# Performance work log

Measured on AMD Instinct MI355X. Metric: run time of the kernel, lower is better.

## Reference

```python
import jax, jax.numpy as jnp
import numpy as np

CODEBOOK_SIZE = 8192
EMBED_DIM = 256


def setup_inputs() -> dict:
    key = jax.random.key(0)
    k1, k2 = jax.random.split(key)
    z = jax.random.normal(k1, (8, 4096, EMBED_DIM), dtype=jnp.float32)
    # matches torch init: uniform_(-1/codebook_size, 1/codebook_size)
    codebook = jax.random.uniform(
        k2, (CODEBOOK_SIZE, EMBED_DIM), dtype=jnp.float32,
        minval=-1.0 / CODEBOOK_SIZE, maxval=1.0 / CODEBOOK_SIZE)
    return {"z": z, "codebook": codebook}


def reference(z, codebook):
    # z: [B, S, D]; codebook: [K, D]
    z_flat = z.reshape(-1, z.shape[-1])                      # [N, D]
    # ||z||^2 - 2 z.E^T + ||E||^2  -> [N, K]
    distances = (
        jnp.sum(z_flat * z_flat, axis=1, keepdims=True)
        - 2.0 * jnp.einsum("nd,kd->nk", z_flat, codebook)
        + jnp.sum(codebook * codebook, axis=1)
    )
    encoding_indices = jnp.argmin(distances, axis=1)         # [N]
    z_q = codebook[encoding_indices].reshape(z.shape)        # [B, S, D]
    return z_q, encoding_indices
```

## Files before the change

### kernel.cpp

```cpp
#include <hip/hip_runtime.h>


#define NROWS 32768
#define DIM   256
#define KCB   8192
#define CANDCAP 128
#define MARGIN  4.5e-4f
#define WBUF    320

#define SB_CAND  0u
#define SB_CNT   8388608u
#define SB_ZSQ   8519680u
#define SB_CSQ   8650752u
#define SB_CSQ1  8683520u
#define SB_OVL   8716288u
#define SB_OVC   8847360u
#define SB_IMG   8847424u
#define SB_NEED  13041728u

using bf16x8 = __attribute__((ext_vector_type(8))) short;
using f32x4  = __attribute__((ext_vector_type(4))) float;

__device__ __forceinline__ unsigned short bf16rne(float f) {
    unsigned u = __float_as_uint(f);
    unsigned r = u + 0x7FFFu + ((u >> 16) & 1u);
    return (unsigned short)(r >> 16);
}

__device__ float np_sumsq_256(const float* __restrict__ p) {
#pragma clang fp contract(off)
    float blk[2];
    #pragma unroll
    for (int b = 0; b < 2; ++b) {
        const float4* q4 = reinterpret_cast<const float4*>(p + b * 128);
        float4 a0 = q4[0], a1 = q4[1];
        float r[8];
        r[0] = __fmul_rn(a0.x, a0.x); r[1] = __fmul_rn(a0.y, a0.y);
        r[2] = __fmul_rn(a0.z, a0.z); r[3] = __fmul_rn(a0.w, a0.w);
        r[4] = __fmul_rn(a1.x, a1.x); r[5] = __fmul_rn(a1.y, a1.y);
        r[6] = __fmul_rn(a1.z, a1.z); r[7] = __fmul_rn(a1.w, a1.w);
        #pragma unroll
        for (int i = 2; i < 32; i += 2) {
            a0 = q4[i]; a1 = q4[i + 1];
            r[0] = __fadd_rn(r[0], __fmul_rn(a0.x, a0.x));
            r[1] = __fadd_rn(r[1], __fmul_rn(a0.y, a0.y));
            r[2] = __fadd_rn(r[2], __fmul_rn(a0.z, a0.z));
            r[3] = __fadd_rn(r[3], __fmul_rn(a0.w, a0.w));
            r[4] = __fadd_rn(r[4], __fmul_rn(a1.x, a1.x));
            r[5] = __fadd_rn(r[5], __fmul_rn(a1.y, a1.y));
            r[6] = __fadd_rn(r[6], __fmul_rn(a1.z, a1.z));
            r[7] = __fadd_rn(r[7], __fmul_rn(a1.w, a1.w));
        }
        blk[b] = __fadd_rn(
            __fadd_rn(__fadd_rn(r[0], r[1]), __fadd_rn(r[2], r[3])),
            __fadd_rn(__fadd_rn(r[4], r[5]), __fadd_rn(r[6], r[7])));
    }
    return __fadd_rn(blk[0], blk[1]);
}

__global__ void vq_prep_kernel(const float* __restrict__ z,
                               const float* __restrict__ cb,
                               char* __restrict__ img,
                               float* __restrict__ zsq, float* __restrict__ csq,
                               float* __restrict__ csq1,
                               unsigned* __restrict__ cnt, unsigned* __restrict__ ovc) {
    int t = blockIdx.x * 256 + threadIdx.x;
    if (t < NROWS) cnt[t] = 0;
    if (t == 0) *ovc = 0;
    if (t < 262144) {
        int s = t & 63, kk = (t >> 6) & 7, T = t >> 9;
        int code = s & 15, lhi = s >> 4;
        const float* src = cb + (size_t)(T * 16 + code) * DIM + kk * 32 + lhi * 8;
        float4 v0 = *reinterpret_cast<const float4*>(src);
        float4 v1 = *reinterpret_cast<const float4*>(src + 4);
        uint4 o;
        o.x = (unsigned)bf16rne(v0.x) | ((unsigned)bf16rne(v0.y) << 16);
        o.y = (unsigned)bf16rne(v0.z) | ((unsigned)bf16rne(v0.w) << 16);
        o.z = (unsigned)bf16rne(v1.x) | ((unsigned)bf16rne(v1.y) << 16);
        o.w = (unsigned)bf16rne(v1.z) | ((unsigned)bf16rne(v1.w) << 16);
        *reinterpret_cast<uint4*>(img + (size_t)T * 8192 + kk * 1024 + s * 16) = o;
    } else if (t < 262144 + KCB) {
        int k = t - 262144;
        float s = np_sumsq_256(cb + (size_t)k * DIM);
        csq[k] = s;
        csq1[k] = s + 1.0f;
    } else if (t < 262144 + KCB + NROWS) {
        int r = t - 262144 - KCB;
        zsq[r] = np_sumsq_256(z + (size_t)r * DIM);
    }
}

__global__ __launch_bounds__(512, 2) void vq_screen_kernel(
    const float* __restrict__ z, const char* __restrict__ img,
    const float* __restrict__ csq1,
    unsigned* __restrict__ cnt, unsigned short* __restrict__ cand) {
    __shared__ unsigned runmin[128];
    __shared__ unsigned wcnt[8];
    __shared__ unsigned wbuf[8][WBUF];
    const int tid = threadIdx.x, lane = tid & 63, wid = tid >> 6;
    const int wr = wid >> 2, wc = wid & 3;
    const int l15 = lane & 15, lhi = lane >> 4;
    const int row0 = blockIdx.x * 128;
    const int tbase = wc * 128;

    bf16x8 ah[4][8];
    #pragma unroll
    for (int m = 0; m < 4; ++m) {
        const float* zr = z + (size_t)(row0 + wr * 64 + m * 16 + l15) * DIM;
        #pragma unroll
        for (int kk = 0; kk < 8; ++kk) {
            float4 v0 = *reinterpret_cast<const float4*>(zr + kk * 32 + lhi * 8);
            float4 v1 = *reinterpret_cast<const float4*>(zr + kk * 32 + lhi * 8 + 4);
            uint4 o;
            o.x = (unsigned)bf16rne(v0.x) | ((unsigned)bf16rne(v0.y) << 16);
            o.y = (unsigned)bf16rne(v0.z) | ((unsigned)bf16rne(v0.w) << 16);
            o.z = (unsigned)bf16rne(v1.x) | ((unsigned)bf16rne(v1.y) << 16);
            o.w = (unsigned)bf16rne(v1.z) | ((unsigned)bf16rne(v1.w) << 16);
            ah[m][kk] = __builtin_bit_cast(bf16x8, o);
        }
    }

    if (tid < 128) runmin[tid] = 0x7F800000u;
    if (tid < 8) wcnt[tid] = 0;
    __syncthreads();

    f32x4 acc[4];
    #pragma unroll
    for (int m = 0; m < 4; ++m) acc[m] = (f32x4){0.f, 0.f, 0.f, 0.f};

    const char*  gp = img + (size_t)tbase * 8192 + (size_t)lane * 16;
    const float* cp = csq1 + tbase * 16 + l15;
    int codeb = tbase * 16 + l15;

    uint4 bA[8]; float csA;
    uint4 bB[8]; float csB;

    auto PUSH = [&](int lr, int code) {
        unsigned pi = atomicAdd(&wcnt[wid], 1u);
        if (pi < WBUF) wbuf[wid][pi] = ((unsigned)lr << 13) | (unsigned)code;
        else {
            int grow = row0 + lr;
            unsigned gs = atomicAdd(&cnt[grow], 1u);
            if (gs < CANDCAP) cand[(size_t)grow * CANDCAP + gs] = (unsigned short)code;
        }
    };

#define CHUNKS(bcur, bnxt, csn, DOLOAD)                                   \
    {                                                                     \
        _Pragma("unroll")                                                 \
        for (int c = 0; c < 4; ++c) {                                     \
            if (DOLOAD) {                                                 \
                bnxt[2*c]   = *reinterpret_cast<const uint4*>(gp + (2*c) * 1024);     \
                bnxt[2*c+1] = *reinterpret_cast<const uint4*>(gp + (2*c+1) * 1024);   \
                if (c == 0) csn = *cp;                                    \
            }                                                             \
            bf16x8 b0 = __builtin_bit_cast(bf16x8, bcur[2*c]);            \
            bf16x8 b1 = __builtin_bit_cast(bf16x8, bcur[2*c+1]);          \
            _Pragma("unroll")                                             \
            for (int m = 0; m < 4; ++m)                                   \
                acc[m] = __builtin_amdgcn_mfma_f32_16x16x32_bf16(ah[m][2*c], b0, acc[m], 0, 0, 0);   \
            _Pragma("unroll")                                             \
            for (int m = 0; m < 4; ++m)                                   \
                acc[m] = __builtin_amdgcn_mfma_f32_16x16x32_bf16(ah[m][2*c+1], b1, acc[m], 0, 0, 0); \
        }                                                                 \
        if (DOLOAD) { gp += 8192; cp += 16; }                             \
    }

#define EPI(csv)                                                          \
    {                                                                     \
        _Pragma("unroll")                                                 \
        for (int m = 0; m < 4; ++m) {                                     \
            const int lr0 = wr * 64 + m * 16 + lhi * 4;                   \
            uint4 rmb = *reinterpret_cast<const uint4*>(&runmin[lr0]);    \
            float s0 = fmaf(acc[m][0], -2.0f, csv);                       \
            float s1 = fmaf(acc[m][1], -2.0f, csv);                       \
            float s2 = fmaf(acc[m][2], -2.0f, csv);                       \
            float s3 = fmaf(acc[m][3], -2.0f, csv);                       \
            bool c0 = s0 < __uint_as_float(rmb.x) + MARGIN;               \
            bool c1 = s1 < __uint_as_float(rmb.y) + MARGIN;               \
            bool c2 = s2 < __uint_as_float(rmb.z) + MARGIN;               \
            bool c3 = s3 < __uint_as_float(rmb.w) + MARGIN;               \
            if (__any(c0 | c1 | c2 | c3)) {                               \
                if (c0) { if (s0 < __uint_as_float(rmb.x)) atomicMin(&runmin[lr0 + 0], __float_as_uint(s0)); PUSH(lr0 + 0, codeb); } \
                if (c1) { if (s1 < __uint_as_float(rmb.y)) atomicMin(&runmin[lr0 + 1], __float_as_uint(s1)); PUSH(lr0 + 1, codeb); } \
                if (c2) { if (s2 < __uint_as_float(rmb.z)) atomicMin(&runmin[lr0 + 2], __float_as_uint(s2)); PUSH(lr0 + 2, codeb); } \
                if (c3) { if (s3 < __uint_as_float(rmb.w)) atomicMin(&runmin[lr0 + 3], __float_as_uint(s3)); PUSH(lr0 + 3, codeb); } \
            }                                                             \
            acc[m] = (f32x4){0.f, 0.f, 0.f, 0.f};                         \
        }                                                                 \
        codeb += 16;                                                      \
    }

    #pragma unroll
    for (int kk = 0; kk < 8; ++kk)
        bA[kk] = *reinterpret_cast<const uint4*>(gp + kk * 1024);
    csA = *cp; gp += 8192; cp += 16;

    CHUNKS(bA, bB, csB, 1);
    {
        #pragma unroll
        for (int m = 0; m < 4; ++m) {
            const int lr0 = wr * 64 + m * 16 + lhi * 4;
            #pragma unroll
            for (int r = 0; r < 4; ++r) {
                float s2 = fmaf(acc[m][r], -2.0f, csA);
                float sm = s2;
                sm = fminf(sm, __shfl_xor(sm, 1));
                sm = fminf(sm, __shfl_xor(sm, 2));
                sm = fminf(sm, __shfl_xor(sm, 4));
                sm = fminf(sm, __shfl_xor(sm, 8));
                if (l15 == 0) atomicMin(&runmin[lr0 + r], __float_as_uint(sm));
                if (s2 < sm + MARGIN) PUSH(lr0 + r, codeb);
            }
            acc[m] = (f32x4){0.f, 0.f, 0.f, 0.f};
        }
        codeb += 16;
    }
    CHUNKS(bB, bA, csA, 1);  EPI(csB);

    for (int t = 2; t < 126; t += 2) {
        CHUNKS(bA, bB, csB, 1);  EPI(csA);
        CHUNKS(bB, bA, csA, 1);  EPI(csB);
    }
    CHUNKS(bA, bB, csB, 1);  EPI(csA);
    CHUNKS(bB, bA, csA, 0);  EPI(csB);

    unsigned n = wcnt[wid]; if (n > WBUF) n = WBUF;
    for (unsigned e = lane; e < n; e += 64) {
        unsigned u = wbuf[wid][e];
        int row = row0 + (int)(u >> 13);
        int code = (int)(u & 8191u);
        unsigned slot = atomicAdd(&cnt[row], 1u);
        if (slot < CANDCAP) cand[(size_t)row * CANDCAP + slot] = (unsigned short)code;
    }
#undef CHUNKS
#undef EPI
}

__global__ __launch_bounds__(256) void vq_exact_kernel(
    const float* __restrict__ z, const float* __restrict__ cb,
    const float* __restrict__ zsq, const float* __restrict__ csq,
    const unsigned* __restrict__ cnt, const unsigned short* __restrict__ cand,
    unsigned* __restrict__ ovl, unsigned* __restrict__ ovc,
    float* __restrict__ idxF, float4* __restrict__ outz, int fused) {
    __shared__ float zrow[4][DIM];
    const int wid = threadIdx.x >> 6, lane = threadIdx.x & 63;
    const int row = blockIdx.x * 4 + wid;

    float4 zv4 = *reinterpret_cast<const float4*>(&z[(size_t)row * DIM + lane * 4]);
    *reinterpret_cast<float4*>(&zrow[wid][lane * 4]) = zv4;
    __syncthreads();

    const unsigned c = cnt[row];
    if (c == 0 || c > CANDCAP) {
        if (lane == 0) { unsigned s = atomicAdd(ovc, 1u); ovl[s] = row; }
        return;
    }

    const float Zr = zsq[row];
    const float4* cb4 = reinterpret_cast<const float4*>(cb);
    float best = 3.4e38f;
    int   bi   = 0x7FFFFFFF;

    for (int j = lane; j < (int)c; j += 64) {
        int k = cand[(size_t)row * CANDCAP + j];
        float a = 0.0f;
        #pragma unroll 8
        for (int q = 0; q < 64; ++q) {
            float4 cv = cb4[(size_t)k * 64 + q];
            float4 zv = *reinterpret_cast<const float4*>(&zrow[wid][q * 4]);
            a = fmaf(zv.x, cv.x, a); a = fmaf(zv.y, cv.y, a);
            a = fmaf(zv.z, cv.z, a); a = fmaf(zv.w, cv.w, a);
        }
        float sv = __fadd_rn(__fsub_rn(Zr, __fmul_rn(2.0f, a)), csq[k]);
        if (sv < best || (sv == best && k < bi)) { best = sv; bi = k; }
    }
    #pragma unroll
    for (int mk = 32; mk >= 1; mk >>= 1) {
        float ov = __shfl_xor(best, mk);
        int   oi = __shfl_xor(bi, mk);
        if (ov < best || (ov == best && oi < bi)) { best = ov; bi = oi; }
    }
    if (lane == 0) idxF[row] = (float)bi;
    if (fused) outz[(size_t)row * 64 + lane] = cb4[(size_t)bi * 64 + lane];
}

__global__ __launch_bounds__(256) void vq_cleanup_kernel(
    const float* __restrict__ z, const float* __restrict__ cb,
    const float* __restrict__ zsq, const float* __restrict__ csq,
    const unsigned* __restrict__ ovl, const unsigned* __restrict__ ovc,
    float* __restrict__ idxF, float4* __restrict__ outz, int fused) {
    __shared__ float zrow[DIM];
    __shared__ float wv[4]; __shared__ int wi[4];
    __shared__ int sbi;
    const int lane = threadIdx.x & 63, wid = threadIdx.x >> 6;
    const unsigned count = *ovc;
    for (unsigned w = blockIdx.x; w < count; w += gridDim.x) {
        const int row = ovl[w];
        __syncthreads();
        *reinterpret_cast<float4*>(&zrow[threadIdx.x * 4 & (DIM - 1)]) =
            *reinterpret_cast<const float4*>(&z[(size_t)row * DIM + (threadIdx.x * 4 & (DIM - 1))]);
        __syncthreads();
        const float Zr = zsq[row];
        const float4* cb4 = reinterpret_cast<const float4*>(cb);
        float best = 3.4e38f; int bi = 0x7FFFFFFF;
        for (int k = threadIdx.x; k < KCB; k += 256) {
            float a = 0.0f;
            #pragma unroll 8
            for (int q = 0; q < 64; ++q) {
                float4 cv = cb4[(size_t)k * 64 + q];
                float4 zv = *reinterpret_cast<const float4*>(&zrow[q * 4]);
                a = fmaf(zv.x, cv.x, a); a = fmaf(zv.y, cv.y, a);
                a = fmaf(zv.z, cv.z, a); a = fmaf(zv.w, cv.w, a);
            }
            float sv = __fadd_rn(__fsub_rn(Zr, __fmul_rn(2.0f, a)), csq[k]);
            if (sv < best || (sv == best && k < bi)) { best = sv; bi = k; }
        }
        #pragma unroll
        for (int mk = 32; mk >= 1; mk >>= 1) {
            float ov = __shfl_xor(best, mk);
            int   oi = __shfl_xor(bi, mk);
            if (ov < best || (ov == best && oi < bi)) { best = ov; bi = oi; }
        }
        if (lane == 0) { wv[wid] = best; wi[wid] = bi; }
        __syncthreads();
        if (threadIdx.x == 0) {
            #pragma unroll
            for (int u = 1; u < 4; ++u)
                if (wv[u] < best || (wv[u] == best && wi[u] < bi)) { best = wv[u]; bi = wi[u]; }
            idxF[row] = (float)bi;
            sbi = bi;
        }
        __syncthreads();
        if (fused && threadIdx.x < 64)
            outz[(size_t)row * 64 + threadIdx.x] = cb4[(size_t)sbi * 64 + threadIdx.x];
    }
}

__global__ void vq_gather_kernel(const float* __restrict__ cb,
                                 const float* __restrict__ idxF,
                                 float4* __restrict__ out4) {
    int g = blockIdx.x * blockDim.x + threadIdx.x;
    const float4* cb4 = reinterpret_cast<const float4*>(cb);
    for (int i = g; i < NROWS * 64; i += gridDim.x * blockDim.x) {
        int row = i >> 6, q = i & 63;
        int idx = (int)idxF[row];
        out4[i] = cb4[(size_t)idx * 64 + q];
    }
}

extern "C" void kernel_launch(void* const* d_in, const int* in_sizes, int n_in,
                              void* d_out, int out_size, void* d_ws, size_t ws_size,
                              hipStream_t stream) {
    const float* z  = (const float*)d_in[0];
    const float* cb = (const float*)d_in[1];
    float* out = (float*)d_out;

    const int fused = (ws_size >= (size_t)SB_NEED) ? 1 : 0;
    char* SB = fused ? (char*)d_ws : (char*)d_out;

    unsigned short* candp = (unsigned short*)(SB + SB_CAND);
    unsigned*       cntp  = (unsigned*)(SB + SB_CNT);
    float*          zsq   = (float*)(SB + SB_ZSQ);
    float*          csq   = (float*)(SB + SB_CSQ);
    float*          csq1  = (float*)(SB + SB_CSQ1);
    unsigned*       ovl   = (unsigned*)(SB + SB_OVL);
    unsigned*       ovc   = (unsigned*)(SB + SB_OVC);
    char*           img   = SB + SB_IMG;
    float*          idxF  = out + 8388608;

    vq_prep_kernel<<<(262144 + KCB + NROWS + 255) / 256, 256, 0, stream>>>(
        z, cb, img, zsq, csq, csq1, cntp, ovc);
    vq_screen_kernel<<<NROWS / 128, 512, 0, stream>>>(z, img, csq1, cntp, candp);
    vq_exact_kernel<<<NROWS / 4, 256, 0, stream>>>(
        z, cb, zsq, csq, cntp, candp, ovl, ovc, idxF, (float4*)out, fused);
    vq_cleanup_kernel<<<64, 256, 0, stream>>>(
        z, cb, zsq, csq, ovl, ovc, idxF, (float4*)out, fused);
    if (!fused)
        vq_gather_kernel<<<2048, 256, 0, stream>>>(cb, idxF, (float4*)out);
}
```

Before: 286.6 us.

## Double-buffer MFMA accumulators to overlap screening epilogue with next tile's MFMAs

The screen kernel's main loop now keeps two accumulator sets and two B-register buffers. Each step issues the MFMAs for one code tile while the epilogue (threshold compare, atomics, candidate push) runs on the previous tile's accumulators, so matrix work can overlap the scalar/LDS epilogue. The csq1 load moves into the epilogue and a bf16 pack helper is factored out. The extra accumulator registers raise VGPR pressure under launch_bounds(512,2) and could cause spilling.

```diff
diff --git a/kernel.cpp b/kernel.cpp
--- a/kernel.cpp
+++ b/kernel.cpp
@@ -20,11 +20,16 @@
 
 using bf16x8 = __attribute__((ext_vector_type(8))) short;
 using f32x4  = __attribute__((ext_vector_type(4))) float;
+using u32x4  = __attribute__((ext_vector_type(4))) unsigned int;
 
 __device__ __forceinline__ unsigned short bf16rne(float f) {
     unsigned u = __float_as_uint(f);
     unsigned r = u + 0x7FFFu + ((u >> 16) & 1u);
     return (unsigned short)(r >> 16);
+}
+
+__device__ __forceinline__ unsigned pack2_bf16(float a, float b) {
+    return (unsigned)bf16rne(a) | ((unsigned)bf16rne(b) << 16);
 }
 
 __device__ float np_sumsq_256(const float* __restrict__ p) {
@@ -74,10 +79,8 @@
         float4 v0 = *reinterpret_cast<const float4*>(src);
         float4 v1 = *reinterpret_cast<const float4*>(src + 4);
         uint4 o;
-        o.x = (unsigned)bf16rne(v0.x) | ((unsigned)bf16rne(v0.y) << 16);
-        o.y = (unsigned)bf16rne(v0.z) | ((unsigned)bf16rne(v0.w) << 16);
-        o.z = (unsigned)bf16rne(v1.x) | ((unsigned)bf16rne(v1.y) << 16);
-        o.w = (unsigned)bf16rne(v1.z) | ((unsigned)bf16rne(v1.w) << 16);
+        o.x = pack2_bf16(v0.x, v0.y); o.y = pack2_bf16(v0.z, v0.w);
+        o.z = pack2_bf16(v1.x, v1.y); o.w = pack2_bf16(v1.z, v1.w);
         *reinterpret_cast<uint4*>(img + (size_t)T * 8192 + kk * 1024 + s * 16) = o;
     } else if (t < 262144 + KCB) {
         int k = t - 262144;
@@ -112,10 +115,8 @@
             float4 v0 = *reinterpret_cast<const float4*>(zr + kk * 32 + lhi * 8);
             float4 v1 = *reinterpret_cast<const float4*>(zr + kk * 32 + lhi * 8 + 4);
             uint4 o;
-            o.x = (unsigned)bf16rne(v0.x) | ((unsigned)bf16rne(v0.y) << 16);
-            o.y = (unsigned)bf16rne(v0.z) | ((unsigned)bf16rne(v0.w) << 16);
-            o.z = (unsigned)bf16rne(v1.x) | ((unsigned)bf16rne(v1.y) << 16);
-            o.w = (unsigned)bf16rne(v1.z) | ((unsigned)bf16rne(v1.w) << 16);
+            o.x = pack2_bf16(v0.x, v0.y); o.y = pack2_bf16(v0.z, v0.w);
+            o.z = pack2_bf16(v1.x, v1.y); o.w = pack2_bf16(v1.z, v1.w);
             ah[m][kk] = __builtin_bit_cast(bf16x8, o);
         }
     }
@@ -124,16 +125,18 @@
     if (tid < 8) wcnt[tid] = 0;
     __syncthreads();
 
-    f32x4 acc[4];
+    f32x4 aA[4], aB[4];
     #pragma unroll
-    for (int m = 0; m < 4; ++m) acc[m] = (f32x4){0.f, 0.f, 0.f, 0.f};
-
-    const char*  gp = img + (size_t)tbase * 8192 + (size_t)lane * 16;
-    const float* cp = csq1 + tbase * 16 + l15;
+    for (int m = 0; m < 4; ++m) {
+        aA[m] = (f32x4){0.f, 0.f, 0.f, 0.f};
+        aB[m] = (f32x4){0.f, 0.f, 0.f, 0.f};
+    }
+
+    const char*  gp  = img + (size_t)tbase * 8192 + (size_t)lane * 16;
+    const float* cpe = csq1 + tbase * 16 + l15;
     int codeb = tbase * 16 + l15;
 
-    uint4 bA[8]; float csA;
-    uint4 bB[8]; float csB;
+    u32x4 bA[8], bB[8];
 
     auto PUSH = [&](int lr, int code) {
         unsigned pi = atomicAdd(&wcnt[wid], 1u);
@@ -145,37 +148,37 @@
         }
     };
 
-#define CHUNKS(bcur, bnxt, csn, DOLOAD)                                   \
+#define LOADR(bh)                                                         \
     {                                                                     \
         _Pragma("unroll")                                                 \
-        for (int c = 0; c < 4; ++c) {                                     \
-            if (DOLOAD) {                                                 \
-                bnxt[2*c]   = *reinterpret_cast<const uint4*>(gp + (2*c) * 1024);     \
-                bnxt[2*c+1] = *reinterpret_cast<const uint4*>(gp + (2*c+1) * 1024);   \
-                if (c == 0) csn = *cp;                                    \
-            }                                                             \
-            bf16x8 b0 = __builtin_bit_cast(bf16x8, bcur[2*c]);            \
-            bf16x8 b1 = __builtin_bit_cast(bf16x8, bcur[2*c+1]);          \
+        for (int kk = 0; kk < 8; ++kk)                                    \
+            bh[kk] = *reinterpret_cast<const u32x4*>(gp + kk * 1024);     \
+        gp += 8192;                                                       \
+    }
+
+#define MFMAS(bh, a)                                                      \
+    {                                                                     \
+        _Pragma("unroll")                                                 \
+        for (int kk = 0; kk < 8; ++kk) {                                  \
+            bf16x8 bv = __builtin_bit_cast(bf16x8, bh[kk]);               \
             _Pragma("unroll")                                             \
             for (int m = 0; m < 4; ++m)                                   \
-                acc[m] = __builtin_amdgcn_mfma_f32_16x16x32_bf16(ah[m][2*c], b0, acc[m], 0, 0, 0);   \
-            _Pragma("unroll")                                             \
-            for (int m = 0; m < 4; ++m)                                   \
-                acc[m] = __builtin_amdgcn_mfma_f32_16x16x32_bf16(ah[m][2*c+1], b1, acc[m], 0, 0, 0); \
+                a[m] = __builtin_amdgcn_mfma_f32_16x16x32_bf16(           \
+                    ah[m][kk], bv, a[m], 0, 0, 0);                        \
         }                                                                 \
-        if (DOLOAD) { gp += 8192; cp += 16; }                             \
-    }
-
-#define EPI(csv)                                                          \
+    }
+
+#define EPI(a)                                                            \
     {                                                                     \
+        const float csv = *cpe; cpe += 16;                                \
         _Pragma("unroll")                                                 \
         for (int m = 0; m < 4; ++m) {                                     \
             const int lr0 = wr * 64 + m * 16 + lhi * 4;                   \
             uint4 rmb = *reinterpret_cast<const uint4*>(&runmin[lr0]);    \
-            float s0 = fmaf(acc[m][0], -2.0f, csv);                       \
-            float s1 = fmaf(acc[m][1], -2.0f, csv);                       \
-            float s2 = fmaf(acc[m][2], -2.0f, csv);                       \
-            float s3 = fmaf(acc[m][3], -2.0f, csv);                       \
+            float s0 = fmaf(a[m][0], -2.0f, csv);                         \
+            float s1 = fmaf(a[m][1], -2.0f, csv);                         \
+            float s2 = fmaf(a[m][2], -2.0f, csv);                         \
+            float s3 = fmaf(a[m][3], -2.0f, csv);                         \
             bool c0 = s0 < __uint_as_float(rmb.x) + MARGIN;               \
             bool c1 = s1 < __uint_as_float(rmb.y) + MARGIN;               \
             bool c2 = s2 < __uint_as_float(rmb.z) + MARGIN;               \
@@ -186,24 +189,24 @@
                 if (c2) { if (s2 < __uint_as_float(rmb.z)) atomicMin(&runmin[lr0 + 2], __float_as_uint(s2)); PUSH(lr0 + 2, codeb); } \
                 if (c3) { if (s3 < __uint_as_float(rmb.w)) atomicMin(&runmin[lr0 + 3], __float_as_uint(s3)); PUSH(lr0 + 3, codeb); } \
             }                                                             \
-            acc[m] = (f32x4){0.f, 0.f, 0.f, 0.f};                         \
+            a[m] = (f32x4){0.f, 0.f, 0.f, 0.f};                           \
         }                                                                 \
         codeb += 16;                                                      \
     }
 
-    #pragma unroll
-    for (int kk = 0; kk < 8; ++kk)
-        bA[kk] = *reinterpret_cast<const uint4*>(gp + kk * 1024);
-    csA = *cp; gp += 8192; cp += 16;
-
-    CHUNKS(bA, bB, csB, 1);
+    LOADR(bA);
+    LOADR(bB);
+    MFMAS(bA, aA);
+    LOADR(bA);
+    MFMAS(bB, aB);
     {
+        const float csv = *cpe; cpe += 16;
         #pragma unroll
         for (int m = 0; m < 4; ++m) {
             const int lr0 = wr * 64 + m * 16 + lhi * 4;
             #pragma unroll
             for (int r = 0; r < 4; ++r) {
-                float s2 = fmaf(acc[m][r], -2.0f, csA);
+                float s2 = fmaf(aA[m][r], -2.0f, csv);
                 float sm = s2;
                 sm = fminf(sm, __shfl_xor(sm, 1));
                 sm = fminf(sm, __shfl_xor(sm, 2));
@@ -212,18 +215,18 @@
                 if (l15 == 0) atomicMin(&runmin[lr0 + r], __float_as_uint(sm));
                 if (s2 < sm + MARGIN) PUSH(lr0 + r, codeb);
             }
-            acc[m] = (f32x4){0.f, 0.f, 0.f, 0.f};
+            aA[m] = (f32x4){0.f, 0.f, 0.f, 0.f};
         }
         codeb += 16;
     }
-    CHUNKS(bB, bA, csA, 1);  EPI(csB);
-
-    for (int t = 2; t < 126; t += 2) {
-        CHUNKS(bA, bB, csB, 1);  EPI(csA);
-        CHUNKS(bB, bA, csA, 1);  EPI(csB);
-    }
-    CHUNKS(bA, bB, csB, 1);  EPI(csA);
-    CHUNKS(bB, bA, csA, 0);  EPI(csB);
+
+    for (int i = 1; i <= 62; ++i) {
+        LOADR(bB);  MFMAS(bA, aA);  EPI(aB);
+        LOADR(bA);  MFMAS(bB, aB);  EPI(aA);
+    }
+    LOADR(bB);  MFMAS(bA, aA);  EPI(aB);
+    MFMAS(bB, aB);  EPI(aA);
+    EPI(aB);
 
     unsigned n = wcnt[wid]; if (n > WBUF) n = WBUF;
     for (unsigned e = lane; e < n; e += 64) {
@@ -233,7 +236,8 @@
         unsigned slot = atomicAdd(&cnt[row], 1u);
         if (slot < CANDCAP) cand[(size_t)row * CANDCAP + slot] = (unsigned short)code;
     }
-#undef CHUNKS
+#undef LOADR
+#undef MFMAS
 #undef EPI
 }
 
```

Result: no change. 292.1 us (+1.9%).
